# Kernel tuning notes

Measured on AMD Instinct MI355X. Metric: run time of the kernel, lower is better.

## Reference

```python
import jax, jax.numpy as jnp
import numpy as np


def _shift(x, k):
    # roll time axis forward by k, zero-filling the first k steps
    if k == 0:
        return x
    return jnp.pad(x, ((0, 0), (k, 0), (0, 0)))[:, : x.shape[1]]


def _stu_conv(u, v, n):
    # u: (B,L,D), v: (L,K) spectral filters; non-tensordot branch of conv()
    B, L, D = u.shape
    K = v.shape[1]
    sgn = jnp.where(jnp.arange(L) % 2 == 1, -1.0, 1.0).astype(jnp.float32)[None, :, None, None]
    ue = jnp.broadcast_to(u[:, :, None, :], (B, L, K, D)).astype(jnp.float32)
    U = jnp.stack([ue, ue * sgn], axis=-1)                     # (B,L,K,D,2)
    Uf = jnp.fft.rfft(U, n=n, axis=1)
    vf = jnp.fft.rfft(v.astype(jnp.float32)[None, :, :, None, None], n=n, axis=1)
    Uc = jnp.fft.irfft(vf * Uf, n=n, axis=1)[:, :L]            # (B,L,K,D,2)
    U_plus = Uc[..., 0]
    U_minus = Uc[..., 1] * sgn
    return U_plus.astype(u.dtype), U_minus.astype(u.dtype)


def setup_inputs() -> dict:
    key = jax.random.key(0)
    ks = jax.random.split(key, 6)
    B, L, D, K, k_u, k_y = 2, 1024, 512, 16, 3, 2
    u = jax.random.normal(ks[0], (B, L, D), jnp.float32)
    filters = jax.random.normal(ks[1], (L, K), jnp.float32) / np.float32(np.sqrt(L))
    M_u = jax.random.normal(ks[2], (D, k_u, D), jnp.float32) * 0.01
    M_y = jax.random.normal(ks[3], (D, k_y, D), jnp.float32) * 0.01
    M_phi_plus = jax.random.normal(ks[4], (K, D, D), jnp.float32) * 0.01
    M_phi_minus = jax.random.normal(ks[5], (K, D, D), jnp.float32) * 0.01
    return {"u": u, "filters": filters, "M_u": M_u, "M_y": M_y,
            "M_phi_plus": M_phi_plus, "M_phi_minus": M_phi_minus}


def reference(u, filters, M_u, M_y, M_phi_plus, M_phi_minus):
    B, L, D = u.shape
    n = 1 << int(np.ceil(np.log2(2 * L - 1)))  # nearest power of two >= 2L-1
    k_u = M_u.shape[1]
    k_y = M_y.shape[1]

    # FFT-based long convolution with the +/- sign trick
    U_plus, U_minus = _stu_conv(u, filters, n)
    spectral = (jnp.einsum('blkd,kdo->blo', U_plus, M_phi_plus)
                + jnp.einsum('blkd,kdo->blo', U_minus, M_phi_minus))

    # input-AR term of compute_ar_strict: sum_j u[t+1-j] @ M_u[:, j-1].T (shifts 0..k_u-1)
    u_sh = jnp.stack([_shift(u, j - 1) for j in range(1, k_u + 1)], axis=1)  # (B,k_u,L,D)
    y_in = jnp.einsum('bjlf,ijf->bli', u_sh, M_u)

    z = spectral + y_in  # (B,L,D)

    # output-AR recurrence of compute_ar_strict as a scan
    def step(y_buf, z_t):
        y_t = z_t + jnp.einsum('bjf,djf->bd', y_buf, M_y)
        y_buf = jnp.concatenate([y_t[:, None], y_buf[:, :-1]], axis=1)
        return y_buf, y_t

    _, ys = jax.lax.scan(step, jnp.zeros((B, k_y, D), z.dtype), jnp.swapaxes(z, 0, 1))
    return jnp.swapaxes(ys, 0, 1)  # (B,L,D)
```

## Files before the change

### kernel.cpp

```cpp
#include <hip/hip_runtime.h>
#include <hip/hip_bf16.h>


using bf16 = __hip_bfloat16;
typedef __attribute__((ext_vector_type(8))) short bf16x8;
typedef __attribute__((ext_vector_type(4))) float f32x4;

#define B_   2
#define L_   1024
#define D_   512
#define K_   16
#define KT   17920
#define ROWS 2048
#define NTAP 6
#define PBLD 3584
#define SPLITD 14
#define SPLITR 6
#define ZBROWS 1032
#define NKS 40
#define NTD 20
#define WZOFF 4194304

#define WAIT_VM6 0x0F76
#define WAIT_VM4 0x0F74
#define WAIT_VM0 0x0F70

__device__ __forceinline__ void gll16(const void* g, void* l) {
    __builtin_amdgcn_global_load_lds(
        (const __attribute__((address_space(1))) unsigned int*)g,
        (__attribute__((address_space(3))) unsigned int*)l, 16, 0, 0);
}

__global__ void prep_all(const float* __restrict__ u, const float* __restrict__ fil,
                         const float* __restrict__ Mu, const float* __restrict__ My,
                         const float* __restrict__ Mp, const float* __restrict__ Mm,
                         bf16* __restrict__ U, bf16* __restrict__ BT,
                         bf16* __restrict__ PB, bf16* __restrict__ W,
                         bf16* __restrict__ Myb, bf16* __restrict__ BTT,
                         bf16* __restrict__ uPT) {
    __shared__ bf16 t[64][72];
    int bid = blockIdx.x, tid = threadIdx.x;
    auto pack4 = [](float4 v) {
        ushort4 o; bf16 h;
        h = __float2bfloat16(v.x); o.x = *(unsigned short*)&h;
        h = __float2bfloat16(v.y); o.y = *(unsigned short*)&h;
        h = __float2bfloat16(v.z); o.z = *(unsigned short*)&h;
        h = __float2bfloat16(v.w); o.w = *(unsigned short*)&h;
        return o;
    };
    if (bid < 3072) {
        int e4 = bid * 256 + tid;
        int r = e4 / 384, rem = e4 % 384;
        int tt = rem >> 7, f = (rem & 127) * 4;
        int b = r >> 10, l = r & 1023;
        float4 v = {0.f, 0.f, 0.f, 0.f};
        if (l >= tt) v = *(const float4*)&u[((size_t)b * L_ + l - tt) * D_ + f];
        *(ushort4*)&U[(size_t)r * KT + 16384 + tt * 512 + f] = pack4(v);
    } else if (bid < 3840) {
        int e4 = (bid - 3072) * 256 + tid;
        int o = e4 / 384, tf4 = (e4 % 384) * 4;
        float4 v = *(const float4*)&Mu[(size_t)o * 1536 + tf4];
        *(ushort4*)&BT[(size_t)o * KT + 16384 + tf4] = pack4(v);
    } else if (bid < 4352) {
        int e4 = (bid - 3840) * 256 + tid;
        int n = e4 >> 8, c4 = (e4 & 255) * 4;
        float4 v;
        if (c4 < 512) {
            v.x = (n == c4) ? 1.f : 0.f;     v.y = (n == c4 + 1) ? 1.f : 0.f;
            v.z = (n == c4 + 2) ? 1.f : 0.f; v.w = (n == c4 + 3) ? 1.f : 0.f;
        } else v = *(const float4*)&My[(size_t)n * 1024 + (c4 - 512)];
        *(ushort4*)&PB[(size_t)n * PBLD + c4] = pack4(v);
    } else if (bid < 5120) {
        int tile = bid - 4352;
        int set = tile >> 8, rem = tile & 255;
        int k = rem >> 4, g = (rem >> 2) & 3, kb = rem & 3;
        for (int idx = tid; idx < 4096; idx += 256) {
            int i = idx >> 5, jp = idx & 31;
            int j = ((jp >> 3) ^ ((i >> 1) & 3)) * 8 + (jp & 7);
            int x = g * 128 + i - kb * 32 - j - (set == 2 ? 1 : 0);
            float v = 0.f;
            if (x >= 0) {
                int row = (set == 0) ? 2 * x : 2 * x + 1;
                v = fil[row * K_ + k];
            }
            W[(size_t)tile * 4096 + idx] = __float2bfloat16(v);
        }
    } else if (bid < 5632) {
        int e4 = (bid - 5120) * 256 + tid;
        float4 v = *(const float4*)&My[(size_t)e4 * 4];
        *(ushort4*)&Myb[(size_t)e4 * 4] = pack4(v);
    } else if (bid < 7872) {
        int tt = bid - 5632;
        int zb = tt >> 6, rem = tt & 63;
        int bx = rem & 7, by = rem >> 3;
        int col = tid & 63, r0 = (tid >> 6) * 16;
        if (zb < 32) {
            int dt = bx * 64, ot = by * 64, c = zb;
            int k = c & 15;
            const float* sp = Mp + (size_t)k * D_ * D_;
            const float* sm = Mm + (size_t)k * D_ * D_;
            float sg = (c < 16) ? 1.f : -1.f;
            for (int i = 0; i < 16; ++i) {
                size_t o_ = (size_t)(dt + r0 + i) * D_ + ot + col;
                t[r0 + i][col] = __float2bfloat16(sp[o_] + sg * sm[o_]);
            }
            __syncthreads();
            for (int i = 0; i < 16; ++i)
                BT[(size_t)(ot + r0 + i) * KT + c * D_ + dt + col] = t[col][r0 + i];
        } else if (zb < 34) {
            int h = zb - 32;
            int dt = bx * 64, ft = by * 64;
            for (int i = 0; i < 16; ++i)
                t[r0 + i][col] = __float2bfloat16(My[(size_t)(dt + r0 + i) * 1024 + (1 - h) * 512 + ft + col]);
            __syncthreads();
            for (int i = 0; i < 16; ++i)
                BTT[(size_t)(ft + r0 + i) * 1024 + h * 512 + dt + col] = t[col][r0 + i];
        } else {
            for (int it = 0; it < 4; ++it) {
                int b = it >> 1, p = it & 1;
                int mt = bx * 64, dt = by * 64;
                __syncthreads();
                for (int i = 0; i < 16; ++i)
                    t[r0 + i][col] = __float2bfloat16(u[((size_t)b * L_ + 2 * (mt + r0 + i) + p) * D_ + dt + col]);
                __syncthreads();
                for (int i = 0; i < 16; ++i)
                    uPT[((size_t)it * 512 + dt + r0 + i) * 512 + mt + col] = t[col][r0 + i];
            }
        }
    } else {
        ushort4 z4 = {0, 0, 0, 0};
        for (int i = 0; i < 4; ++i)
            *(ushort4*)&W[(size_t)WZOFF + (size_t)(i * 256 + tid) * 4] = z4;
    }
}

__device__ __forceinline__ void phi_body(
    const bf16* A, int lda, const bf16* BT, int ldb,
    bf16* out, int ldo, int klen, const bf16* add, int lad,
    int row0, int col0, bf16* sA, bf16* sB)
{
    const int tid = threadIdx.x, lane = tid & 63, wave = tid >> 6;
    const int wm = (wave & 1) * 64, wn = (wave >> 1) * 64;
    const int ml = lane & 15, q = lane >> 4;
    const int srow = lane >> 2, scol = (((lane & 3) ^ ((srow >> 1) & 3))) * 8;
    const int swz = ((ml >> 1) & 3);
    f32x4 acc[4][4] = {};

    for (int k = 0; k < klen; k += 32) {
        __syncthreads();
        #pragma unroll
        for (int repi = 0; repi < 2; ++repi) {
            int a = wave + repi * 4;
            gll16(A  + (size_t)(row0 + a * 16 + srow) * lda + k + scol, &sA[a * 512]);
            gll16(BT + (size_t)(col0 + a * 16 + srow) * ldb + k + scol, &sB[a * 512]);
        }
        __syncthreads();
        bf16x8 af[4], bfr[4];
        #pragma unroll
        for (int i = 0; i < 4; ++i)
            af[i] = *(const bf16x8*)&sA[(wm + i * 16 + ml) * 32 + (q ^ swz) * 8];
        #pragma unroll
        for (int j = 0; j < 4; ++j)
            bfr[j] = *(const bf16x8*)&sB[(wn + j * 16 + ml) * 32 + (q ^ swz) * 8];
        #pragma unroll
        for (int i = 0; i < 4; ++i)
            #pragma unroll
            for (int j = 0; j < 4; ++j)
                acc[i][j] = __builtin_amdgcn_mfma_f32_16x16x32_bf16(af[i], bfr[j], acc[i][j], 0, 0, 0);
    }
    #pragma unroll
    for (int i = 0; i < 4; ++i)
        #pragma unroll
        for (int j = 0; j < 4; ++j)
            #pragma unroll
            for (int reg = 0; reg < 4; ++reg) {
                int r = row0 + wm + i * 16 + q * 4 + reg;
                int cc = col0 + wn + j * 16 + ml;
                float v = acc[i][j][reg];
                if (add) v += __bfloat162float(add[(size_t)r * lad + cc]);
                out[(size_t)r * ldo + cc] = __float2bfloat16(v);
            }
}

__device__ __forceinline__ void phi_body8(
    const bf16* A, int lda, const bf16* BT, int ldb,
    bf16* out, int ldo, int klen, const bf16* add, int lad,
    int row0, int col0, bf16* sA, bf16* sB)
{
    const int tid = threadIdx.x, lane = tid & 63, wave = tid >> 6;
    const int wm = (wave & 1) * 64, wn = (wave >> 1) * 64;
    const int ml = lane & 15, q = lane >> 4;
    const int srow = lane >> 2, scol = (((lane & 3) ^ ((srow >> 1) & 3))) * 8;
    const int swz = ((ml >> 1) & 3);
    f32x4 acc[4][4] = {};

    for (int k = 0; k < klen; k += 32) {
        __syncthreads();
        gll16(A  + (size_t)(row0 + wave * 16 + srow) * lda + k + scol, &sA[wave * 512]);
        gll16(BT + (size_t)(col0 + (2 * wave) * 16 + srow) * ldb + k + scol, &sB[(2 * wave) * 512]);
        gll16(BT + (size_t)(col0 + (2 * wave + 1) * 16 + srow) * ldb + k + scol, &sB[(2 * wave + 1) * 512]);
        __syncthreads();
        bf16x8 af[4], bfr[4];
        #pragma unroll
        for (int i = 0; i < 4; ++i)
            af[i] = *(const bf16x8*)&sA[(wm + i * 16 + ml) * 32 + (q ^ swz) * 8];
        #pragma unroll
        for (int j = 0; j < 4; ++j)
            bfr[j] = *(const bf16x8*)&sB[(wn + j * 16 + ml) * 32 + (q ^ swz) * 8];
        #pragma unroll
        for (int i = 0; i < 4; ++i)
            #pragma unroll
            for (int j = 0; j < 4; ++j)
                acc[i][j] = __builtin_amdgcn_mfma_f32_16x16x32_bf16(af[i], bfr[j], acc[i][j], 0, 0, 0);
    }
    #pragma unroll
    for (int i = 0; i < 4; ++i)
        #pragma unroll
        for (int j = 0; j < 4; ++j)
            #pragma unroll
            for (int reg = 0; reg < 4; ++reg) {
                int r = row0 + wm + i * 16 + q * 4 + reg;
                int cc = col0 + wn + j * 16 + ml;
                float v = acc[i][j][reg];
                if (add) v += __bfloat162float(add[(size_t)r * lad + cc]);
                out[(size_t)r * ldo + cc] = __float2bfloat16(v);
            }
}

__device__ __forceinline__ void mmtile_pipe(
    const bf16* Abase, int lda, const bf16* Bbase, int ldb, int n,
    bf16* o, int ldo, int row0, int col0, bf16 (*sA)[4096], bf16 (*sB)[4096])
{
    const int tid = threadIdx.x, lane = tid & 63, wave = tid >> 6;
    const int wm = (wave & 1) * 64, wn = (wave >> 1) * 64;
    const int ml = lane & 15, q = lane >> 4;
    const int srow = lane >> 2, scol = (((lane & 3) ^ ((srow >> 1) & 3))) * 8;
    const int swz = ((ml >> 1) & 3);
    f32x4 acc[4][4] = {};

    const bf16* bA0 = Abase + (size_t)(wave * 16 + srow) * lda + scol;
    const bf16* bA1 = Abase + (size_t)((wave + 4) * 16 + srow) * lda + scol;
    const bf16* bB0 = Bbase + (size_t)(wave * 16 + srow) * ldb + scol;
    const bf16* bB1 = Bbase + (size_t)((wave + 4) * 16 + srow) * ldb + scol;
    auto stage = [&](int s, int buf) {
        gll16(bA0 + s * 32, &sA[buf][wave * 512]);
        gll16(bA1 + s * 32, &sA[buf][(wave + 4) * 512]);
        gll16(bB0 + s * 32, &sB[buf][wave * 512]);
        gll16(bB1 + s * 32, &sB[buf][(wave + 4) * 512]);
    };
    auto compute = [&](int c) {
        bf16x8 af[4], bfr[4];
        #pragma unroll
        for (int i = 0; i < 4; ++i)
            af[i] = *(const bf16x8*)&sA[c][(wm + i * 16 + ml) * 32 + (q ^ swz) * 8];
        #pragma unroll
        for (int j = 0; j < 4; ++j)
            bfr[j] = *(const bf16x8*)&sB[c][(wn + j * 16 + ml) * 32 + (q ^ swz) * 8];
        #pragma unroll
        for (int i = 0; i < 4; ++i)
            #pragma unroll
            for (int j = 0; j < 4; ++j)
                acc[i][j] = __builtin_amdgcn_mfma_f32_16x16x32_bf16(af[i], bfr[j], acc[i][j], 0, 0, 0);
    };
    stage(0, 0); stage(1, 1);
    int c = 0, nb = 2;
    for (int i = 0; i < n - 1; ++i) {
        __builtin_amdgcn_s_waitcnt(WAIT_VM4);
        __builtin_amdgcn_s_barrier();
        if (i + 2 < n) stage(i + 2, nb);
        compute(c);
        c = (c == 2) ? 0 : c + 1; nb = (nb == 2) ? 0 : nb + 1;
    }
    __builtin_amdgcn_s_waitcnt(WAIT_VM0);
    __builtin_amdgcn_s_barrier();
    compute(c);

    #pragma unroll
    for (int i = 0; i < 4; ++i)
        #pragma unroll
        for (int j = 0; j < 4; ++j)
            #pragma unroll
            for (int reg = 0; reg < 4; ++reg) {
                int r = row0 + wm + i * 16 + q * 4 + reg;
                int cc = col0 + wn + j * 16 + ml;
                o[(size_t)r * ldo + cc] = __float2bfloat16(acc[i][j][reg]);
            }
}

__global__ void k_ztaps(const bf16* __restrict__ partD, float* __restrict__ z,
                        bf16* __restrict__ zbuf, bf16* PB, const bf16* BTT) {
    __shared__ bf16 sA[3][4096];
    __shared__ bf16 sB[3][4096];
    int bid = blockIdx.x;
    if (bid < 32) {
        int row0 = (bid & 3) * 128, col0 = (bid >> 2) * 128;
        mmtile_pipe(PB + 3 * 512 + (size_t)row0 * PBLD, PBLD,
                    BTT + (size_t)col0 * 1024, 1024, 32,
                    PB + 5 * 512, PBLD, row0, col0, sA, sB);
        return;
    }
    if (bid == 32) {
        ushort4 z4 = {0, 0, 0, 0};
        for (int i = 0; i < 8; ++i) {
            int e4 = i * 256 + threadIdx.x;
            int b = e4 >> 10, rem = e4 & 1023;
            int g = rem >> 7, c4 = (rem & 127) * 4;
            *(ushort4*)&zbuf[(size_t)(b * ZBROWS + g) * 512 + c4] = z4;
        }
        return;
    }
    int t = (bid - 33) * 256 + threadIdx.x;
    int r = t >> 7, f4 = (t & 127) * 4;
    const ushort4* p = (const ushort4*)partD;
    float4 s = {0.f, 0.f, 0.f, 0.f};
    #pragma unroll
    for (int c = 0; c < SPLITD; ++c) {
        ushort4 v = p[(size_t)c * (ROWS * D_ / 4) + t];
        s.x += __uint_as_float((unsigned)v.x << 16);
        s.y += __uint_as_float((unsigned)v.y << 16);
        s.z += __uint_as_float((unsigned)v.z << 16);
        s.w += __uint_as_float((unsigned)v.w << 16);
    }
    ((float4*)z)[t] = s;
    ushort4 zb4;
    { bf16 h;
      h = __float2bfloat16(s.x); zb4.x = *(unsigned short*)&h;
      h = __float2bfloat16(s.y); zb4.y = *(unsigned short*)&h;
      h = __float2bfloat16(s.z); zb4.z = *(unsigned short*)&h;
      h = __float2bfloat16(s.w); zb4.w = *(unsigned short*)&h; }
    int b = r >> 10, li = r & 1023;
    *(ushort4*)&zbuf[(size_t)(b * ZBROWS + 8 + li) * 512 + f4] = zb4;
}

__global__ void reduce_out(const float* __restrict__ z, const bf16* __restrict__ partR,
                           float* __restrict__ out) {
    int t = blockIdx.x * 256 + threadIdx.x;
    if (t >= ROWS * D_ / 4) return;
    float4 s = ((const float4*)z)[t];
    const ushort4* p = (const ushort4*)partR;
    #pragma unroll
    for (int c = 0; c < SPLITR; ++c) {
        ushort4 v = p[(size_t)c * (ROWS * D_ / 4) + t];
        s.x += __uint_as_float((unsigned)v.x << 16);
        s.y += __uint_as_float((unsigned)v.y << 16);
        s.z += __uint_as_float((unsigned)v.z << 16);
        s.w += __uint_as_float((unsigned)v.w << 16);
    }
    ((float4*)out)[t] = s;
}

__global__ __launch_bounds__(512, 2) void conv8(
    const bf16* __restrict__ W, const bf16* __restrict__ uPT,
    bf16* __restrict__ U,
    const bf16* PB, const bf16* BTT, const bf16* Myb)
{
    __shared__ bf16 sA[4][8192];
    __shared__ bf16 sB[4][8192];
    int id = blockIdx.x;
    const int tid = threadIdx.x, lane = tid & 63, wave = tid >> 6;
    if (id < 24) {
        int pz = id >> 3, sub = id & 7;
        int row0 = (sub & 3) * 128, col0 = (sub >> 2) * 256;
        bf16* BTTw = (bf16*)BTT; bf16* PBw = (bf16*)PB;
        if (pz == 0)
            phi_body8(PB, PBLD, BTT, 1024, PBw + 2 * 512, PBLD, 1024,
                      nullptr, 0, row0, col0, &sA[0][0], &sB[0][0]);
        else if (pz == 1)
            phi_body8(BTT + 512, 1024, Myb + 512, 1024,
                      BTTw + (size_t)512 * 1024, 1024, 512,
                      nullptr, 0, row0, col0, &sA[0][0], &sB[0][0]);
        else
            phi_body8(BTT + 512, 1024, Myb, 1024,
                      BTTw + (size_t)512 * 1024 + 512, 1024, 512,
                      BTT, 1024, row0, col0, &sA[0][0], &sB[0][0]);
        return;
    }
    const int cid = id - 24;
    const int mt2 = (cid < 256) ? 1 : 0;
    const int m = cid & 255;
    const int xcd8 = m & 7, slot = m >> 3;
    const int plane = xcd8 >> 1, dt2 = xcd8 & 1;
    const int pc = (plane & 1) | ((slot & 1) << 1);
    const int k = slot >> 1;
    const int b = plane >> 1;
    const int p = (pc & 1) ^ (pc >> 1);
    const int set = (pc < 2) ? 0 : (pc == 2 ? 1 : 2);
    const int ch = (pc < 2) ? k : 16 + k;
    const int nks = (mt2 + 1) * 8;
    const int NT = nks >> 1;

    const int wm = (wave >> 2) * 128;
    const int wn = (wave & 3) * 64;
    const int ml = lane & 15, q16 = lane >> 4;
    const int srow = lane >> 2, scol = (((lane & 3) ^ ((srow >> 1) & 3))) * 8;
    const int swz = ((ml >> 1) & 3);
    const int koff = (q16 ^ swz) * 8;

    const int a0 = 2 * wave, a1 = a0 + 1;
    const int rb = mt2 * 2 + (a0 >> 3);
    const bf16* wbase = W + ((size_t)(set * 16 + k) * 16) * 4096;
    const bf16* wzero = W + (size_t)WZOFF;
    const bf16* bB0 = uPT + ((size_t)plane * 512 + dt2 * 256 + a0 * 16 + srow) * 512 + scol;
    const bf16* bB1 = uPT + ((size_t)plane * 512 + dt2 * 256 + a1 * 16 + srow) * 512 + scol;

    auto stageA = [&](int s) {
        if (s >= nks) return;
        int s4 = s >> 2;
        const bf16* t0 = (rb >= s4)
            ? wbase + (size_t)((rb - s4) * 4 + (s & 3)) * 4096 : wzero;
        gll16(t0 + ((a0 & 7) * 512 + lane * 8), &sA[s & 3][a0 * 512]);
        gll16(t0 + ((a1 & 7) * 512 + lane * 8), &sA[s & 3][a1 * 512]);
    };
    auto stageB = [&](int s) {
        if (s >= nks) return;
        gll16(bB0 + s * 32, &sB[s & 3][a0 * 512]);
        gll16(bB1 + s * 32, &sB[s & 3][a1 * 512]);
    };

    f32x4 acc[8][4] = {};

    stageB(0); stageB(1); stageA(0); stageA(1);
    stageB(2); stageB(3); stageA(2);
    __builtin_amdgcn_s_waitcnt(WAIT_VM6);
    __builtin_amdgcn_s_barrier();

    for (int t = 0; t < NT; ++t) {
        const int u0 = (2 * t) & 3, u1 = u0 + 1;
        bf16x8 bfr[4][2];
        #pragma unroll
        for (int ph = 0; ph < 4; ++ph) {
            bf16x8 af[2][2];
            if (ph == 0) {
                #pragma unroll
                for (int fc = 0; fc < 4; ++fc) {
                    bfr[fc][0] = *(const bf16x8*)&sB[u0][(wn + fc * 16 + ml) * 32 + koff];
                    bfr[fc][1] = *(const bf16x8*)&sB[u1][(wn + fc * 16 + ml) * 32 + koff];
                }
            }
            #pragma unroll
            for (int f2 = 0; f2 < 2; ++f2) {
                int R = wm + (2 * ph + f2) * 16 + ml;
                af[f2][0] = *(const bf16x8*)&sA[u0][R * 32 + koff];
                af[f2][1] = *(const bf16x8*)&sA[u1][R * 32 + koff];
            }
            if (ph == 0)      stageA(2 * t + 3);
            else if (ph == 1) stageB(2 * t + 4);
            else if (ph == 2) stageB(2 * t + 5);
            else              stageA(2 * t + 4);
            __builtin_amdgcn_s_barrier();
            __builtin_amdgcn_s_setprio(1);
            #pragma unroll
            for (int f2 = 0; f2 < 2; ++f2)
                #pragma unroll
                for (int fc = 0; fc < 4; ++fc) {
                    acc[2 * ph + f2][fc] = __builtin_amdgcn_mfma_f32_16x16x32_bf16(
                        af[f2][0], bfr[fc][0], acc[2 * ph + f2][fc], 0, 0, 0);
                    acc[2 * ph + f2][fc] = __builtin_amdgcn_mfma_f32_16x16x32_bf16(
                        af[f2][1], bfr[fc][1], acc[2 * ph + f2][fc], 0, 0, 0);
                }
            __builtin_amdgcn_s_setprio(0);
            if (ph == 3) {
                if (t < NT - 2)       __builtin_amdgcn_s_waitcnt(WAIT_VM6);
                else if (t == NT - 2) __builtin_amdgcn_s_waitcnt(WAIT_VM0);
            }
            __builtin_amdgcn_s_barrier();
        }
    }

    #pragma unroll
    for (int i = 0; i < 8; ++i)
        #pragma unroll
        for (int j = 0; j < 4; ++j)
            #pragma unroll
            for (int reg = 0; reg < 4; ++reg) {
                int mm = mt2 * 256 + wm + i * 16 + q16 * 4 + reg;
                int l = 2 * mm + p;
                int d = dt2 * 256 + wn + j * 16 + ml;
                U[(size_t)(b * L_ + l) * KT + ch * 512 + d] = __float2bfloat16(acc[i][j][reg]);
            }
}

__global__ __launch_bounds__(512, 2) void gemm_d(
    const bf16* __restrict__ U, const bf16* __restrict__ BT,
    bf16* __restrict__ part, const bf16* PB, const bf16* BTT)
{
    __shared__ bf16 sA[4][8192];
    __shared__ bf16 sB[4][8192];
    int id = blockIdx.x;
    const int tid = threadIdx.x, lane = tid & 63, wave = tid >> 6;
    if (id < 32) {
        if (wave >= 4) {
            for (int i = 0; i < 64; ++i) __syncthreads();
            return;
        }
        int r0_ = (id & 3) * 128, c0_ = (id >> 2) * 128;
        phi_body(PB + 512, PBLD, BTT, 1024, (bf16*)PB + 3 * 512, PBLD, 1024,
                 nullptr, 0, r0_, c0_, &sA[0][0], &sB[0][0]);
        return;
    }
    id -= 32;
    const int xsw = id & 7, slot = id >> 3;
    const int w_ = xsw * 28 + slot;
    const int g = w_ >> 3, rtile = w_ & 7;
    const int zz = g >> 1;
    const int row0 = rtile * 256, col0 = (g & 1) * 256;
    const int k0 = zz * (KT / SPLITD);

    const int wm = (wave >> 2) * 128;
    const int wn = (wave & 3) * 64;
    const int ml = lane & 15, q16 = lane >> 4;
    const int srow = lane >> 2, scol = (((lane & 3) ^ ((srow >> 1) & 3))) * 8;
    const int swz = ((ml >> 1) & 3);
    const int koff = (q16 ^ swz) * 8;

    const int a0 = 2 * wave, a1 = 2 * wave + 1;
    const bf16* bA0 = U  + (size_t)(row0 + a0 * 16 + srow) * KT + k0 + scol;
    const bf16* bA1 = U  + (size_t)(row0 + a1 * 16 + srow) * KT + k0 + scol;
    const bf16* bB0 = BT + (size_t)(col0 + a0 * 16 + srow) * KT + k0 + scol;
    const bf16* bB1 = BT + (size_t)(col0 + a1 * 16 + srow) * KT + k0 + scol;
    auto stageA = [&](int s) {
        if (s >= NKS) return;
        gll16(bA0 + s * 32, &sA[s & 3][a0 * 512]);
        gll16(bA1 + s * 32, &sA[s & 3][a1 * 512]);
    };
    auto stageB = [&](int s) {
        if (s >= NKS) return;
        gll16(bB0 + s * 32, &sB[s & 3][a0 * 512]);
        gll16(bB1 + s * 32, &sB[s & 3][a1 * 512]);
    };

    f32x4 acc[8][4] = {};

    stageB(0); stageB(1); stageA(0); stageA(1);
    stageB(2); stageB(3); stageA(2);
    __builtin_amdgcn_s_waitcnt(WAIT_VM6);
    __builtin_amdgcn_s_barrier();

    for (int t = 0; t < NTD; ++t) {
        const int u0 = (2 * t) & 3, u1 = u0 + 1;
        bf16x8 bfr[4][2];
        #pragma unroll
        for (int ph = 0; ph < 4; ++ph) {
            bf16x8 af[2][2];
            if (ph == 0) {
                #pragma unroll
                for (int fc = 0; fc < 4; ++fc) {
                    bfr[fc][0] = *(const bf16x8*)&sB[u0][(wn + fc * 16 + ml) * 32 + koff];
                    bfr[fc][1] = *(const bf16x8*)&sB[u1][(wn + fc * 16 + ml) * 32 + koff];
                }
            }
            #pragma unroll
            for (int f2 = 0; f2 < 2; ++f2) {
                int R = wm + (2 * ph + f2) * 16 + ml;
                af[f2][0] = *(const bf16x8*)&sA[u0][R * 32 + koff];
                af[f2][1] = *(const bf16x8*)&sA[u1][R * 32 + koff];
            }
            if (ph == 0)      stageA(2 * t + 3);
            else if (ph == 1) stageB(2 * t + 4);
            else if (ph == 2) stageB(2 * t + 5);
            else              stageA(2 * t + 4);
            __builtin_amdgcn_s_barrier();
            __builtin_amdgcn_s_setprio(1);
            #pragma unroll
            for (int f2 = 0; f2 < 2; ++f2)
                #pragma unroll
                for (int fc = 0; fc < 4; ++fc) {
                    acc[2 * ph + f2][fc] = __builtin_amdgcn_mfma_f32_16x16x32_bf16(
                        af[f2][0], bfr[fc][0], acc[2 * ph + f2][fc], 0, 0, 0);
                    acc[2 * ph + f2][fc] = __builtin_amdgcn_mfma_f32_16x16x32_bf16(
                        af[f2][1], bfr[fc][1], acc[2 * ph + f2][fc], 0, 0, 0);
                }
            __builtin_amdgcn_s_setprio(0);
            if (ph == 3) {
                if (t < NTD - 2)       __builtin_amdgcn_s_waitcnt(WAIT_VM6);
                else if (t == NTD - 2) __builtin_amdgcn_s_waitcnt(WAIT_VM0);
            }
            __builtin_amdgcn_s_barrier();
        }
    }

    bf16* o = part + (size_t)zz * ROWS * D_;
    #pragma unroll
    for (int i = 0; i < 8; ++i)
        #pragma unroll
        for (int j = 0; j < 4; ++j)
            #pragma unroll
            for (int reg = 0; reg < 4; ++reg) {
                int r = row0 + wm + i * 16 + q16 * 4 + reg;
                int cc = col0 + wn + j * 16 + ml;
                o[(size_t)r * D_ + cc] = __float2bfloat16(acc[i][j][reg]);
            }
}

__global__ __launch_bounds__(256, 3) void gemm_r(
    const bf16* __restrict__ zbuf, const bf16* __restrict__ BT,
    bf16* __restrict__ part)
{
    __shared__ bf16 sA[3][4096];
    __shared__ bf16 sB[3][4096];
    const int row0 = blockIdx.x * 128, col0 = blockIdx.y * 128;
    const int zz = blockIdx.z;
    const int s = 1 + zz;
    const int b = row0 >> 10, li0 = row0 & 1023;
    mmtile_pipe(zbuf + ((size_t)(b * ZBROWS + 8 + li0 - s)) * 512, 512,
                BT + (size_t)col0 * PBLD + (size_t)zz * 512, PBLD,
                16, part + (size_t)zz * ROWS * D_, D_, row0, col0, sA, sB);
}

extern "C" void kernel_launch(void* const* d_in, const int* in_sizes, int n_in,
                              void* d_out, int out_size, void* d_ws, size_t ws_size,
                              hipStream_t stream) {
    const float* u   = (const float*)d_in[0];
    const float* fil = (const float*)d_in[1];
    const float* Mu  = (const float*)d_in[2];
    const float* My  = (const float*)d_in[3];
    const float* Mp  = (const float*)d_in[4];
    const float* Mm  = (const float*)d_in[5];
    float* out = (float*)d_out;

    char* ws = (char*)d_ws;
    size_t off = 0;
    auto alloc = [&](size_t bytes) { void* p = ws + off; off = (off + bytes + 255) & ~(size_t)255; return p; };
    bf16*  U    = (bf16*) alloc((size_t)ROWS * KT * 2);
    bf16*  BT   = (bf16*) alloc((size_t)512 * KT * 2);
    bf16*  PB   = (bf16*) alloc((size_t)512 * PBLD * 2);
    bf16*  BTT  = (bf16*) alloc((size_t)1024 * 1024 * 2);
    bf16*  Myb  = (bf16*) alloc((size_t)512 * 1024 * 2);
    float* z    = (float*)alloc((size_t)ROWS * D_ * 4);
    bf16*  zb   = (bf16*) alloc((size_t)B_ * ZBROWS * 512 * 2);
    char*  region = (char*)alloc((size_t)16 * ROWS * D_ * 2);
    bf16*  W    = (bf16*)region;
    bf16*  uPT  = (bf16*)(region + (size_t)768 * 4096 * 2);
    bf16*  partD = (bf16*)region;
    bf16*  partR = (bf16*)region;

    prep_all<<<7873, 256, 0, stream>>>(u, fil, Mu, My, Mp, Mm,
                                       U, BT, PB, W, Myb, BTT, uPT);

    conv8<<<536, 512, 0, stream>>>(W, uPT, U, PB, BTT, Myb);

    gemm_d<<<256, 512, 0, stream>>>(U, BT, partD, PB, BTT);

    k_ztaps<<<1057, 256, 0, stream>>>(partD, z, zb, PB, BTT);

    gemm_r<<<dim3(16, 4, SPLITR), 256, 0, stream>>>(zb, PB + 512, partR);

    reduce_out<<<(ROWS * D_ / 4 + 255) / 256, 256, 0, stream>>>(z, partR, out);
}
```

Measured before the change: 229.7 us.

## Merge conv8 tile passes per block and pipeline phi side-GEMMs with triple buffering

The conv8 grid shrinks from 536 to 256 blocks. Each block now runs both row-tile passes (mt2=1 then mt2=0) in turn, and the first 24 blocks also run a phi side-GEMM before their conv work instead of being separate blocks. The phi GEMM loop changes from a synchronous load-then-compute loop to a 3-stage global_load_lds pipeline with counted waits. This aims to cut the tail and scheduling imbalance and to hide load latency in the phi GEMMs. The cost is that the 24 blocks carrying phi work get longer, which may lengthen the critical path.

```diff
diff --git a/kernel.cpp b/kernel.cpp
--- a/kernel.cpp
+++ b/kernel.cpp
@@ -23,6 +23,7 @@
 
 #define WAIT_VM6 0x0F76
 #define WAIT_VM4 0x0F74
+#define WAIT_VM3 0x0F73
 #define WAIT_VM0 0x0F70
 
 __device__ __forceinline__ void gll16(const void* g, void* l) {
@@ -182,10 +183,10 @@
             }
 }
 
-__device__ __forceinline__ void phi_body8(
+__device__ __forceinline__ void phi_pipe8(
     const bf16* A, int lda, const bf16* BT, int ldb,
     bf16* out, int ldo, int klen, const bf16* add, int lad,
-    int row0, int col0, bf16* sA, bf16* sB)
+    int row0, int col0, bf16* sAr, bf16* sBr)
 {
     const int tid = threadIdx.x, lane = tid & 63, wave = tid >> 6;
     const int wm = (wave & 1) * 64, wn = (wave >> 1) * 64;
@@ -194,25 +195,42 @@
     const int swz = ((ml >> 1) & 3);
     f32x4 acc[4][4] = {};
 
-    for (int k = 0; k < klen; k += 32) {
-        __syncthreads();
-        gll16(A  + (size_t)(row0 + wave * 16 + srow) * lda + k + scol, &sA[wave * 512]);
-        gll16(BT + (size_t)(col0 + (2 * wave) * 16 + srow) * ldb + k + scol, &sB[(2 * wave) * 512]);
-        gll16(BT + (size_t)(col0 + (2 * wave + 1) * 16 + srow) * ldb + k + scol, &sB[(2 * wave + 1) * 512]);
-        __syncthreads();
+    const bf16* bA  = A  + (size_t)(row0 + wave * 16 + srow) * lda + scol;
+    const bf16* bB0 = BT + (size_t)(col0 + (2 * wave) * 16 + srow) * ldb + scol;
+    const bf16* bB1 = BT + (size_t)(col0 + (2 * wave + 1) * 16 + srow) * ldb + scol;
+    auto stage = [&](int s, int buf) {
+        gll16(bA  + s * 32, &sAr[buf * 4096 + wave * 512]);
+        gll16(bB0 + s * 32, &sBr[buf * 8192 + (2 * wave) * 512]);
+        gll16(bB1 + s * 32, &sBr[buf * 8192 + (2 * wave + 1) * 512]);
+    };
+    auto compute = [&](int c) {
         bf16x8 af[4], bfr[4];
         #pragma unroll
         for (int i = 0; i < 4; ++i)
-            af[i] = *(const bf16x8*)&sA[(wm + i * 16 + ml) * 32 + (q ^ swz) * 8];
+            af[i] = *(const bf16x8*)&sAr[c * 4096 + (wm + i * 16 + ml) * 32 + (q ^ swz) * 8];
         #pragma unroll
         for (int j = 0; j < 4; ++j)
-            bfr[j] = *(const bf16x8*)&sB[(wn + j * 16 + ml) * 32 + (q ^ swz) * 8];
+            bfr[j] = *(const bf16x8*)&sBr[c * 8192 + (wn + j * 16 + ml) * 32 + (q ^ swz) * 8];
         #pragma unroll
         for (int i = 0; i < 4; ++i)
             #pragma unroll
             for (int j = 0; j < 4; ++j)
                 acc[i][j] = __builtin_amdgcn_mfma_f32_16x16x32_bf16(af[i], bfr[j], acc[i][j], 0, 0, 0);
-    }
+    };
+    const int n = klen >> 5;
+    stage(0, 0); stage(1, 1);
+    int c = 0, nb = 2;
+    for (int i = 0; i < n - 1; ++i) {
+        __builtin_amdgcn_s_waitcnt(WAIT_VM3);
+        __builtin_amdgcn_s_barrier();
+        if (i + 2 < n) stage(i + 2, nb);
+        compute(c);
+        c = (c == 2) ? 0 : c + 1; nb = (nb == 2) ? 0 : nb + 1;
+    }
+    __builtin_amdgcn_s_waitcnt(WAIT_VM0);
+    __builtin_amdgcn_s_barrier();
+    compute(c);
+
     #pragma unroll
     for (int i = 0; i < 4; ++i)
         #pragma unroll
@@ -363,22 +381,20 @@
         int row0 = (sub & 3) * 128, col0 = (sub >> 2) * 256;
         bf16* BTTw = (bf16*)BTT; bf16* PBw = (bf16*)PB;
         if (pz == 0)
-            phi_body8(PB, PBLD, BTT, 1024, PBw + 2 * 512, PBLD, 1024,
+            phi_pipe8(PB, PBLD, BTT, 1024, PBw + 2 * 512, PBLD, 1024,
                       nullptr, 0, row0, col0, &sA[0][0], &sB[0][0]);
         else if (pz == 1)
-            phi_body8(BTT + 512, 1024, Myb + 512, 1024,
+            phi_pipe8(BTT + 512, 1024, Myb + 512, 1024,
                       BTTw + (size_t)512 * 1024, 1024, 512,
                       nullptr, 0, row0, col0, &sA[0][0], &sB[0][0]);
         else
-            phi_body8(BTT + 512, 1024, Myb, 1024,
+            phi_pipe8(BTT + 512, 1024, Myb, 1024,
                       BTTw + (size_t)512 * 1024 + 512, 1024, 512,
                       BTT, 1024, row0, col0, &sA[0][0], &sB[0][0]);
-        return;
-    }
-    const int cid = id - 24;
-    const int mt2 = (cid < 256) ? 1 : 0;
-    const int m = cid & 255;
-    const int xcd8 = m & 7, slot = m >> 3;
+        __syncthreads();
+    }
+    const int cid = id;
+    const int xcd8 = cid & 7, slot = cid >> 3;
     const int plane = xcd8 >> 1, dt2 = xcd8 & 1;
     const int pc = (plane & 1) | ((slot & 1) << 1);
     const int k = slot >> 1;
@@ -386,8 +402,6 @@
     const int p = (pc & 1) ^ (pc >> 1);
     const int set = (pc < 2) ? 0 : (pc == 2 ? 1 : 2);
     const int ch = (pc < 2) ? k : 16 + k;
-    const int nks = (mt2 + 1) * 8;
-    const int NT = nks >> 1;
 
     const int wm = (wave >> 2) * 128;
     const int wn = (wave & 3) * 64;
@@ -397,87 +411,95 @@
     const int koff = (q16 ^ swz) * 8;
 
     const int a0 = 2 * wave, a1 = a0 + 1;
-    const int rb = mt2 * 2 + (a0 >> 3);
     const bf16* wbase = W + ((size_t)(set * 16 + k) * 16) * 4096;
     const bf16* wzero = W + (size_t)WZOFF;
     const bf16* bB0 = uPT + ((size_t)plane * 512 + dt2 * 256 + a0 * 16 + srow) * 512 + scol;
     const bf16* bB1 = uPT + ((size_t)plane * 512 + dt2 * 256 + a1 * 16 + srow) * 512 + scol;
 
-    auto stageA = [&](int s) {
-        if (s >= nks) return;
-        int s4 = s >> 2;
-        const bf16* t0 = (rb >= s4)
-            ? wbase + (size_t)((rb - s4) * 4 + (s & 3)) * 4096 : wzero;
-        gll16(t0 + ((a0 & 7) * 512 + lane * 8), &sA[s & 3][a0 * 512]);
-        gll16(t0 + ((a1 & 7) * 512 + lane * 8), &sA[s & 3][a1 * 512]);
-    };
-    auto stageB = [&](int s) {
-        if (s >= nks) return;
-        gll16(bB0 + s * 32, &sB[s & 3][a0 * 512]);
-        gll16(bB1 + s * 32, &sB[s & 3][a1 * 512]);
-    };
-
-    f32x4 acc[8][4] = {};
-
-    stageB(0); stageB(1); stageA(0); stageA(1);
-    stageB(2); stageB(3); stageA(2);
-    __builtin_amdgcn_s_waitcnt(WAIT_VM6);
-    __builtin_amdgcn_s_barrier();
-
-    for (int t = 0; t < NT; ++t) {
-        const int u0 = (2 * t) & 3, u1 = u0 + 1;
-        bf16x8 bfr[4][2];
-        #pragma unroll
-        for (int ph = 0; ph < 4; ++ph) {
-            bf16x8 af[2][2];
-            if (ph == 0) {
+    auto do_pass = [&](int mt2p) {
+        const int nks = (mt2p + 1) * 8;
+        const int NT = nks >> 1;
+        const int rb = mt2p * 2 + (a0 >> 3);
+
+        auto stageA = [&](int s) {
+            if (s >= nks) return;
+            int s4 = s >> 2;
+            const bf16* t0 = (rb >= s4)
+                ? wbase + (size_t)((rb - s4) * 4 + (s & 3)) * 4096 : wzero;
+            gll16(t0 + ((a0 & 7) * 512 + lane * 8), &sA[s & 3][a0 * 512]);
+            gll16(t0 + ((a1 & 7) * 512 + lane * 8), &sA[s & 3][a1 * 512]);
+        };
+        auto stageB = [&](int s) {
+            if (s >= nks) return;
+            gll16(bB0 + s * 32, &sB[s & 3][a0 * 512]);
+            gll16(bB1 + s * 32, &sB[s & 3][a1 * 512]);
+        };
+
+        f32x4 acc[8][4] = {};
+
+        stageB(0); stageB(1); stageA(0); stageA(1);
+        stageB(2); stageB(3); stageA(2);
+        __builtin_amdgcn_s_waitcnt(WAIT_VM6);
+        __builtin_amdgcn_s_barrier();
+
+        for (int t = 0; t < NT; ++t) {
+            const int u0 = (2 * t) & 3, u1 = u0 + 1;
+            bf16x8 bfr[4][2];
+            #pragma unroll
+            for (int ph = 0; ph < 4; ++ph) {
+                bf16x8 af[2][2];
+                if (ph == 0) {
+                    #pragma unroll
+                    for (int fc = 0; fc < 4; ++fc) {
+                        bfr[fc][0] = *(const bf16x8*)&sB[u0][(wn + fc * 16 + ml) * 32 + koff];
+                        bfr[fc][1] = *(const bf16x8*)&sB[u1][(wn + fc * 16 + ml) * 32 + koff];
+                    }
+                }
                 #pragma unroll
-                for (int fc = 0; fc < 4; ++fc) {
-                    bfr[fc][0] = *(const bf16x8*)&sB[u0][(wn + fc * 16 + ml) * 32 + koff];
-                    bfr[fc][1] = *(const bf16x8*)&sB[u1][(wn + fc * 16 + ml) * 32 + koff];
+                for (int f2 = 0; f2 < 2; ++f2) {
+                    int R = wm + (2 * ph + f2) * 16 + ml;
+                    af[f2][0] = *(const bf16x8*)&sA[u0][R * 32 + koff];
+                    af[f2][1] = *(const bf16x8*)&sA[u1][R * 32 + koff];
                 }
-            }
-            #pragma unroll
-            for (int f2 = 0; f2 < 2; ++f2) {
-                int R = wm + (2 * ph + f2) * 16 + ml;
-                af[f2][0] = *(const bf16x8*)&sA[u0][R * 32 + koff];
-                af[f2][1] = *(const bf16x8*)&sA[u1][R * 32 + koff];
-            }
-            if (ph == 0)      stageA(2 * t + 3);
-            else if (ph == 1) stageB(2 * t + 4);
-            else if (ph == 2) stageB(2 * t + 5);
-            else              stageA(2 * t + 4);
-            __builtin_amdgcn_s_barrier();
-            __builtin_amdgcn_s_setprio(1);
-            #pragma unroll
-            for (int f2 = 0; f2 < 2; ++f2)
+                if (ph == 0)      stageA(2 * t + 3);
+                else if (ph == 1) stageB(2 * t + 4);
+                else if (ph == 2) stageB(2 * t + 5);
+                else              stageA(2 * t + 4);
+                __builtin_amdgcn_s_barrier();
+                __builtin_amdgcn_s_setprio(1);
                 #pragma unroll
-                for (int fc = 0; fc < 4; ++fc) {
-                    acc[2 * ph + f2][fc] = __builtin_amdgcn_mfma_f32_16x16x32_bf16(
-                        af[f2][0], bfr[fc][0], acc[2 * ph + f2][fc], 0, 0, 0);
-                    acc[2 * ph + f2][fc] = __builtin_amdgcn_mfma_f32_16x16x32_bf16(
-                        af[f2][1], bfr[fc][1], acc[2 * ph + f2][fc], 0, 0, 0);
+                for (int f2 = 0; f2 < 2; ++f2)
+                    #pragma unroll
+                    for (int fc = 0; fc < 4; ++fc) {
+                        acc[2 * ph + f2][fc] = __builtin_amdgcn_mfma_f32_16x16x32_bf16(
+                            af[f2][0], bfr[fc][0], acc[2 * ph + f2][fc], 0, 0, 0);
+                        acc[2 * ph + f2][fc] = __builtin_amdgcn_mfma_f32_16x16x32_bf16(
+                            af[f2][1], bfr[fc][1], acc[2 * ph + f2][fc], 0, 0, 0);
+                    }
+                __builtin_amdgcn_s_setprio(0);
+                if (ph == 3) {
+                    if (t < NT - 2)       __builtin_amdgcn_s_waitcnt(WAIT_VM6);
+                    else if (t == NT - 2) __builtin_amdgcn_s_waitcnt(WAIT_VM0);
                 }
-            __builtin_amdgcn_s_setprio(0);
-            if (ph == 3) {
-                if (t < NT - 2)       __builtin_amdgcn_s_waitcnt(WAIT_VM6);
-                else if (t == NT - 2) __builtin_amdgcn_s_waitcnt(WAIT_VM0);
-            }
-            __builtin_amdgcn_s_barrier();
+                __builtin_amdgcn_s_barrier();
+            }
         }
-    }
-
-    #pragma unroll
-    for (int i = 0; i < 8; ++i)
-        #pragma unroll
-        for (int j = 0; j < 4; ++j)
-            #pragma unroll
-            for (int reg = 0; reg < 4; ++reg) {
-                int mm = mt2 * 256 + wm + i * 16 + q16 * 4 + reg;
-                int l = 2 * mm + p;
-                int d = dt2 * 256 + wn + j * 16 + ml;
-                U[(size_t)(b * L_ + l) * KT + ch * 512 + d] = __float2bfloat16(acc[i][j][reg]);
-            }
+
+        #pragma unroll
+        for (int i = 0; i < 8; ++i)
+            #pragma unroll
+            for (int j = 0; j < 4; ++j)
+                #pragma unroll
+                for (int reg = 0; reg < 4; ++reg) {
+                    int mm = mt2p * 256 + wm + i * 16 + q16 * 4 + reg;
+                    int l = 2 * mm + p;
+                    int d = dt2 * 256 + wn + j * 16 + ml;
+                    U[(size_t)(b * L_ + l) * KT + ch * 512 + d] = __float2bfloat16(acc[i][j][reg]);
+                }
+    };
+
+    do_pass(1);
+    do_pass(0);
 }
 
 __global__ __launch_bounds__(512, 2) void gemm_d(
@@ -637,7 +659,7 @@
     prep_all<<<7873, 256, 0, stream>>>(u, fil, Mu, My, Mp, Mm,
                                        U, BT, PB, W, Myb, BTT, uPT);
 
-    conv8<<<536, 512, 0, stream>>>(W, uPT, U, PB, BTT, Myb);
+    conv8<<<256, 512, 0, stream>>>(W, uPT, U, PB, BTT, Myb);
 
     gemm_d<<<256, 512, 0, stream>>>(U, BT, partD, PB, BTT);
 
```

After: 250.0 us. +8.8%, slower.
